# Optimization experiments

Measured on AMD Instinct MI355X. Metric: run time of the kernel, lower is better.

## Reference

```python
import jax, jax.numpy as jnp
import numpy as np

N_HEAD = 32
N_KV_HEAD = 8
HEAD_DIM = 64
N_EMBD = 2048
B, T = 2, 2048
ROPE_BASE = 10000.0


def _rope_cos_sin(T, head_dim, dtype):
    pos = jnp.arange(T, dtype=jnp.float32)
    dim_arr = jnp.arange(0, head_dim, 2, dtype=jnp.float32)
    freqs = ROPE_BASE ** (-dim_arr / head_dim)
    theta = jnp.outer(pos, freqs)                      # [T, hd/2]
    cos = jnp.concatenate([jnp.cos(theta), jnp.cos(theta)], axis=-1)  # [T, hd]
    sin = jnp.concatenate([jnp.sin(theta), jnp.sin(theta)], axis=-1)
    # broadcast to [1, T, 1, hd]
    return cos[None, :, None, :].astype(dtype), sin[None, :, None, :].astype(dtype)


def _rotate_half(v):
    h = v.shape[-1] // 2
    return jnp.concatenate([-v[..., h:], v[..., :h]], axis=-1)


def setup_inputs() -> dict:
    key = jax.random.key(0)
    kx, kq, kk, kv, ko = jax.random.split(key, 5)
    s = 1.0 / np.sqrt(N_EMBD)
    return {
        "x": jax.random.normal(kx, (B, T, N_EMBD), dtype=jnp.float32),
        "wq": jax.random.normal(kq, (N_EMBD, N_HEAD * HEAD_DIM), dtype=jnp.float32) * s,
        "wk": jax.random.normal(kk, (N_EMBD, N_KV_HEAD * HEAD_DIM), dtype=jnp.float32) * s,
        "wv": jax.random.normal(kv, (N_EMBD, N_KV_HEAD * HEAD_DIM), dtype=jnp.float32) * s,
        "wo": jax.random.normal(ko, (N_HEAD * HEAD_DIM, N_EMBD), dtype=jnp.float32) * s,
    }


def reference(x, wq, wk, wv, wo):
    Bx, Tx, C = x.shape
    n_rep = N_HEAD // N_KV_HEAD

    xq = (x @ wq).reshape(Bx, Tx, N_HEAD, HEAD_DIM)
    xk = (x @ wk).reshape(Bx, Tx, N_KV_HEAD, HEAD_DIM)
    xv = (x @ wv).reshape(Bx, Tx, N_KV_HEAD, HEAD_DIM)

    cos, sin = _rope_cos_sin(Tx, HEAD_DIM, x.dtype)
    xq = xq * cos + _rotate_half(xq) * sin
    xk = xk * cos + _rotate_half(xk) * sin

    # GQA: repeat_interleave KV heads to match query heads
    xk = jnp.repeat(xk, n_rep, axis=2)  # [B, T, H, hd]
    xv = jnp.repeat(xv, n_rep, axis=2)

    scale = 1.0 / np.sqrt(HEAD_DIM)
    # scores: [B, H, T, T]
    scores = jnp.einsum("bqhd,bkhd->bhqk", xq, xk) * scale
    causal = jnp.tril(jnp.ones((Tx, Tx), dtype=bool))
    scores = jnp.where(causal[None, None], scores, -jnp.inf)
    probs = jax.nn.softmax(scores, axis=-1)

    out = jnp.einsum("bhqk,bkhd->bqhd", probs, xv).reshape(Bx, Tx, N_HEAD * HEAD_DIM)
    return out @ wo
```

## Files before the change

kernel.cpp:

```cpp
#include <hip/hip_runtime.h>
#include <hip/hip_bf16.h>
#include <cstdint>
#include <cstddef>

#define B_ 2
#define T_ 2048
#define H_ 32
#define KVH_ 8
#define D_ 64
#define C_ 2048
#define NQKV 3072

typedef short short8 __attribute__((ext_vector_type(8)));
typedef float f32x4 __attribute__((ext_vector_type(4)));
typedef unsigned short u16;

__device__ __forceinline__ u16 f2b(float f) {
  union { float f; unsigned u; } x; x.f = f;
  unsigned r = x.u + 0x7fffu + ((x.u >> 16) & 1u);
  return (u16)(r >> 16);
}

__device__ __forceinline__ void gload16(const void* g, void* l) {
  __builtin_amdgcn_global_load_lds(
      (const __attribute__((address_space(1))) unsigned int*)g,
      (__attribute__((address_space(3))) unsigned int*)l,
      16, 0, 0);
}

__device__ __forceinline__ f32x4 mfma16(short8 a, short8 b, f32x4 c) {
  return __builtin_amdgcn_mfma_f32_16x16x32_bf16(a, b, c, 0, 0, 0);
}

__device__ __forceinline__ unsigned cvtpk(float lo_, float hi_) {
  unsigned r;
  asm("v_cvt_pk_bf16_f32 %0, %1, %2" : "=v"(r) : "v"(lo_), "v"(hi_));
  return r;
}

__global__ void k_tbl(float* __restrict__ tbl) {
  int i = blockIdx.x * 256 + threadIdx.x;
  int t = i >> 5, f = i & 31;
  double freq = pow(10000.0, -(double)f / 32.0);
  double th = (double)t * freq;
  tbl[i * 2 + 0] = (float)cos(th);
  tbl[i * 2 + 1] = (float)sin(th);
}

__global__ void k_cvtx(const float* __restrict__ x, u16* __restrict__ xb) {
  int i = blockIdx.x * 256 + threadIdx.x;
  float4 v = ((const float4*)x)[i];
  ushort4 o;
  o.x = f2b(v.x); o.y = f2b(v.y); o.z = f2b(v.z); o.w = f2b(v.w);
  ((ushort4*)xb)[i] = o;
}

__global__ void k_transw_qkv(const float* __restrict__ wq, const float* __restrict__ wk,
                             const float* __restrict__ wv, u16* __restrict__ dst) {
  __shared__ float t[32][33];
  int tx = threadIdx.x, ty = threadIdx.y;
  int k0 = blockIdx.y * 32, n0g = blockIdx.x * 32;
  const float* src;
  int N, col0;
  if (n0g < 2048)      { src = wq; N = 2048; col0 = n0g; }
  else if (n0g < 2560) { src = wk; N = 512;  col0 = n0g - 2048; }
  else                 { src = wv; N = 512;  col0 = n0g - 2560; }
#pragma unroll
  for (int i = 0; i < 4; i++)
    t[ty + i * 8][tx] = src[(size_t)(k0 + ty + i * 8) * N + col0 + tx];
  __syncthreads();
#pragma unroll
  for (int i = 0; i < 4; i++) {
    int nl = ty + i * 8;
    dst[(size_t)(n0g + nl) * 2048 + k0 + tx] = f2b(t[tx][nl]);
  }
}

__global__ void k_transw(const float* __restrict__ src, u16* __restrict__ dst, int N) {
  __shared__ float t[32][33];
  int tx = threadIdx.x, ty = threadIdx.y;
  int k0 = blockIdx.y * 32, n0 = blockIdx.x * 32;
#pragma unroll
  for (int i = 0; i < 4; i++)
    t[ty + i * 8][tx] = src[(size_t)(k0 + ty + i * 8) * N + n0 + tx];
  __syncthreads();
#pragma unroll
  for (int i = 0; i < 4; i++) {
    int nl = ty + i * 8;
    dst[(size_t)(n0 + nl) * 2048 + k0 + tx] = f2b(t[tx][nl]);
  }
}

template <int MODE>
__global__ __launch_bounds__(256, 2) void k_gemm(const u16* __restrict__ A,
                                                 const u16* __restrict__ Bt,
                                                 void* __restrict__ Cc,
                                                 int M, int N, int K,
                                                 const float* __restrict__ tbl,
                                                 u16* __restrict__ Qb,
                                                 u16* __restrict__ Kb,
                                                 u16* __restrict__ Vt) {
  __shared__ __align__(16) u16 As[128 * 64];
  __shared__ __align__(16) u16 Bs[128 * 64];
  const int tid = threadIdx.x;
  const int w = tid >> 6, l = tid & 63;
  const int lo = l & 15, hi = l >> 4;
  const int m0 = blockIdx.y * 128, n0 = blockIdx.x * 128;
  const int wr = w >> 1, wc = w & 1;
  f32x4 acc[4][4];
#pragma unroll
  for (int i = 0; i < 4; i++)
#pragma unroll
    for (int j = 0; j < 4; j++) acc[i][j] = (f32x4){0.f, 0.f, 0.f, 0.f};

  for (int k0 = 0; k0 < K; k0 += 64) {
#pragma unroll
    for (int i = 0; i < 4; i++) {
      int cid = i * 256 + tid;
      int row = cid >> 3, kc = cid & 7;
      gload16(A + (size_t)(m0 + row) * K + k0 + kc * 8, &As[(i * 256 + w * 64) * 8]);
      gload16(Bt + (size_t)(n0 + row) * K + k0 + kc * 8, &Bs[(i * 256 + w * 64) * 8]);
    }
    __syncthreads();
#pragma unroll
    for (int kk = 0; kk < 2; kk++) {
      short8 a[4], b[4];
#pragma unroll
      for (int i = 0; i < 4; i++)
        a[i] = *(const short8*)&As[(wr * 64 + i * 16 + lo) * 64 + kk * 32 + hi * 8];
#pragma unroll
      for (int j = 0; j < 4; j++)
        b[j] = *(const short8*)&Bs[(wc * 64 + j * 16 + lo) * 64 + kk * 32 + hi * 8];
#pragma unroll
      for (int i = 0; i < 4; i++)
#pragma unroll
        for (int j = 0; j < 4; j++) acc[i][j] = mfma16(a[i], b[j], acc[i][j]);
    }
    __syncthreads();
  }
  const int r0 = m0 + wr * 64, c0 = n0 + wc * 64;

  if (MODE == 0) {
#pragma unroll
    for (int i = 0; i < 4; i++)
#pragma unroll
      for (int j = 0; j < 4; j++) {
        f32x4 v = acc[i][j];
        int col = c0 + j * 16 + lo;
        int rw = r0 + i * 16 + hi * 4;
#pragma unroll
        for (int r = 0; r < 4; r++)
          ((float*)Cc)[(size_t)(rw + r) * N + col] = v[r];
      }
  } else {
    const int hd = c0 >> 6;
    const int b = m0 >> 11;
    if (hd < 40) {
      const bool isQ = (hd < 32);
      const float sc = isQ ? 0.125f * 1.44269504089f : 1.0f;
      u16* dst = isQ ? (Qb + (size_t)(b * H_ + hd) * T_ * 64)
                     : (Kb + (size_t)(b * KVH_ + (hd - 32)) * T_ * 64);
#pragma unroll
      for (int i = 0; i < 4; i++)
#pragma unroll
        for (int r = 0; r < 4; r++) {
          int t = (r0 + i * 16 + hi * 4 + r) & (T_ - 1);
          float2 cA = *(const float2*)&tbl[((size_t)t * 32 + lo) * 2];
          float2 cB = *(const float2*)&tbl[((size_t)t * 32 + 16 + lo) * 2];
          float a0 = acc[i][0][r], a1 = acc[i][1][r];
          float a2 = acc[i][2][r], a3 = acc[i][3][r];
          size_t rb = (size_t)t * 64;
          dst[rb + lo]      = f2b((a0 * cA.x - a2 * cA.y) * sc);
          dst[rb + 32 + lo] = f2b((a2 * cA.x + a0 * cA.y) * sc);
          dst[rb + 16 + lo] = f2b((a1 * cB.x - a3 * cB.y) * sc);
          dst[rb + 48 + lo] = f2b((a3 * cB.x + a1 * cB.y) * sc);
        }
    } else {
      const int kvh = hd - 40;
      u16* dst = Vt + (size_t)(b * KVH_ + kvh) * 64 * T_;
#pragma unroll
      for (int i = 0; i < 4; i++)
#pragma unroll
        for (int j = 0; j < 4; j++) {
          int t = (r0 + i * 16 + hi * 4) & (T_ - 1);
          int dd = j * 16 + lo;
          f32x4 v = acc[i][j];
          ushort4 ov;
          ov.x = f2b(v[0]); ov.y = f2b(v[1]); ov.z = f2b(v[2]); ov.w = f2b(v[3]);
          *(ushort4*)&dst[(size_t)dd * T_ + t] = ov;
        }
    }
  }
}

#define PSTR 40
__global__ __launch_bounds__(256)
__attribute__((amdgpu_waves_per_eu(3, 3)))
void k_attn(const u16* __restrict__ Qb,
            const u16* __restrict__ Kb,
            const u16* __restrict__ Vt,
            u16* __restrict__ Ob) {
  __shared__ __align__(16) u16 Pl[4][2][16 * PSTR];
  const int tid = threadIdx.x, w = tid >> 6, l = tid & 63;
  const int lo = l & 15, hi = l >> 4;
  const int b = blockIdx.z, h = blockIdx.y, kvh = h >> 2;
  const int p = (int)blockIdx.x * 4 + w;

  const size_t qbase = (size_t)(b * H_ + h) * T_ * 64;
  const size_t kbase = (size_t)(b * KVH_ + kvh) * T_ * 64;
  const size_t vbase = (size_t)(b * KVH_ + kvh) * 64 * T_;

  auto LOADK = [&](short8 (&ak)[2][2], int kv0) {
#pragma unroll
    for (int f = 0; f < 2; f++)
#pragma unroll
      for (int hf = 0; hf < 2; hf++)
        ak[f][hf] = *(const short8*)&Kb[kbase + (size_t)(kv0 + f * 16 + lo) * 64 + hf * 32 + hi * 8];
  };

  for (int pass = 0; pass < 2; pass++) {
    const int tile = pass ? (63 - p) : p;
    const int q0 = tile * 32;

    short8 aq[2][2];
#pragma unroll
    for (int qt = 0; qt < 2; qt++)
#pragma unroll
      for (int hf = 0; hf < 2; hf++)
        aq[qt][hf] = *(const short8*)&Qb[qbase + (size_t)(q0 + qt * 16 + lo) * 64 + hf * 32 + hi * 8];

    f32x4 o[2][4];
    float m[2], lsum[2];
#pragma unroll
    for (int qt = 0; qt < 2; qt++) {
      m[qt] = -1e30f; lsum[qt] = 0.f;
#pragma unroll
      for (int jd = 0; jd < 4; jd++) o[qt][jd] = (f32x4){0.f, 0.f, 0.f, 0.f};
    }

    auto STEP = [&](const short8 (&ak)[2][2], int kv0, bool masked) {
      short8 av[4];
#pragma unroll
      for (int jd = 0; jd < 4; jd++)
        av[jd] = *(const short8*)&Vt[vbase + (size_t)(jd * 16 + lo) * T_ + kv0 + hi * 8];

      f32x4 s[2][2];
      __builtin_amdgcn_s_setprio(1);
#pragma unroll
      for (int qt = 0; qt < 2; qt++)
#pragma unroll
        for (int f = 0; f < 2; f++) {
          f32x4 acc = (f32x4){0.f, 0.f, 0.f, 0.f};
          acc = mfma16(ak[f][0], aq[qt][0], acc);
          acc = mfma16(ak[f][1], aq[qt][1], acc);
          s[qt][f] = acc;
        }
      __builtin_amdgcn_s_setprio(0);

#pragma unroll
      for (int qt = 0; qt < 2; qt++) {
        const int myq = q0 + qt * 16 + lo;
        float p_[8];
#pragma unroll
        for (int f = 0; f < 2; f++)
#pragma unroll
          for (int r = 0; r < 4; r++) {
            float v = s[qt][f][r];
            if (masked) {
              int kv = kv0 + f * 16 + hi * 4 + r;
              v = (kv <= myq) ? v : -1e30f;
            }
            p_[f * 4 + r] = v;
          }
        float mx = fmaxf(fmaxf(fmaxf(p_[0], p_[1]), fmaxf(p_[2], p_[3])),
                         fmaxf(fmaxf(p_[4], p_[5]), fmaxf(p_[6], p_[7])));
        mx = fmaxf(mx, __shfl_xor(mx, 16));
        mx = fmaxf(mx, __shfl_xor(mx, 32));
        if (!__all(mx <= m[qt] + 11.5f)) {
          float mn = fmaxf(m[qt], mx);
          float a_ = exp2f(m[qt] - mn);
          m[qt] = mn;
          lsum[qt] *= a_;
#pragma unroll
          for (int jd = 0; jd < 4; jd++) {
            f32x4 t = o[qt][jd];
#pragma unroll
            for (int r = 0; r < 4; r++) t[r] *= a_;
            o[qt][jd] = t;
          }
        }
        float sm = 0.f;
#pragma unroll
        for (int i = 0; i < 8; i++) { p_[i] = exp2f(p_[i] - m[qt]); sm += p_[i]; }
        sm += __shfl_xor(sm, 16);
        sm += __shfl_xor(sm, 32);
        lsum[qt] += sm;
        uint2 w0, w1;
        w0.x = cvtpk(p_[0], p_[1]); w0.y = cvtpk(p_[2], p_[3]);
        w1.x = cvtpk(p_[4], p_[5]); w1.y = cvtpk(p_[6], p_[7]);
        *(uint2*)&Pl[w][qt][lo * PSTR + hi * 4] = w0;
        *(uint2*)&Pl[w][qt][lo * PSTR + 16 + hi * 4] = w1;
      }

#pragma unroll
      for (int qt = 0; qt < 2; qt++) {
        short8 pb = *(const short8*)&Pl[w][qt][lo * PSTR + hi * 8];
        __builtin_amdgcn_s_setprio(1);
#pragma unroll
        for (int jd = 0; jd < 4; jd++) o[qt][jd] = mfma16(av[jd], pb, o[qt][jd]);
        __builtin_amdgcn_s_setprio(0);
      }
    };

    short8 akA[2][2], akB[2][2];
    LOADK(akA, 0);
    int kv0 = 0;
    while (kv0 + 64 <= q0) {
      LOADK(akB, kv0 + 32);
      STEP(akA, kv0, false);
      LOADK(akA, kv0 + 64);
      STEP(akB, kv0 + 32, false);
      kv0 += 64;
    }
    if (kv0 < q0) {
      LOADK(akB, q0);
      STEP(akA, kv0, false);
      STEP(akB, q0, true);
    } else {
      STEP(akA, q0, true);
    }

#pragma unroll
    for (int qt = 0; qt < 2; qt++) {
      const int myq = q0 + qt * 16 + lo;
      float inv = 1.0f / lsum[qt];
      size_t obase = ((size_t)(b * T_ + myq) * H_ + h) * 64;
#pragma unroll
      for (int jd = 0; jd < 4; jd++) {
        ushort4 ov;
        ov.x = f2b(o[qt][jd][0] * inv);
        ov.y = f2b(o[qt][jd][1] * inv);
        ov.z = f2b(o[qt][jd][2] * inv);
        ov.w = f2b(o[qt][jd][3] * inv);
        *(ushort4*)&Ob[obase + jd * 16 + hi * 4] = ov;
      }
    }
  }
}

constexpr size_t OFF_TBL = 0;
constexpr size_t SZ_TBL = (size_t)T_ * 32 * 2 * 4;
constexpr size_t OFF_XB = OFF_TBL + SZ_TBL;
constexpr size_t SZ_XB = (size_t)B_ * T_ * C_ * 2;
constexpr size_t OFF_WQKVT = OFF_XB + SZ_XB;
constexpr size_t SZ_WQKVT = (size_t)NQKV * C_ * 2;
constexpr size_t OFF_WOT = OFF_WQKVT + SZ_WQKVT;
constexpr size_t SZ_WOT = (size_t)C_ * C_ * 2;
constexpr size_t OFF_QB = OFF_WOT + SZ_WOT;
constexpr size_t SZ_QB = (size_t)B_ * H_ * T_ * D_ * 2;
constexpr size_t OFF_KB = OFF_QB + SZ_QB;
constexpr size_t SZ_KVB = (size_t)B_ * KVH_ * T_ * D_ * 2;
constexpr size_t OFF_VT = OFF_KB + SZ_KVB;
constexpr size_t OFF_OB = OFF_VT + SZ_KVB;
constexpr size_t SZ_OB = (size_t)B_ * T_ * H_ * D_ * 2;

extern "C" void kernel_launch(void* const* d_in, const int* in_sizes, int n_in,
                              void* d_out, int out_size, void* d_ws, size_t ws_size,
                              hipStream_t stream) {
  const float* x = (const float*)d_in[0];
  const float* wq = (const float*)d_in[1];
  const float* wk = (const float*)d_in[2];
  const float* wv = (const float*)d_in[3];
  const float* wo = (const float*)d_in[4];

  char* ws = (char*)d_ws;
  float* tbl = (float*)(ws + OFF_TBL);
  u16* xb = (u16*)(ws + OFF_XB);
  u16* wqkvT = (u16*)(ws + OFF_WQKVT);
  u16* woT = (u16*)(ws + OFF_WOT);
  u16* Qb = (u16*)(ws + OFF_QB);
  u16* Kb = (u16*)(ws + OFF_KB);
  u16* Vt = (u16*)(ws + OFF_VT);
  u16* Ob = (u16*)(ws + OFF_OB);

  k_tbl<<<256, 256, 0, stream>>>(tbl);
  k_cvtx<<<8192, 256, 0, stream>>>(x, xb);
  dim3 tb(32, 8);
  k_transw_qkv<<<dim3(96, 64), tb, 0, stream>>>(wq, wk, wv, wqkvT);
  k_transw<<<dim3(64, 64), tb, 0, stream>>>(wo, woT, 2048);

  k_gemm<1><<<dim3(NQKV / 128, (B_ * T_) / 128), 256, 0, stream>>>(
      xb, wqkvT, nullptr, B_ * T_, NQKV, C_, tbl, Qb, Kb, Vt);
  k_attn<<<dim3(8, H_, B_), 256, 0, stream>>>(Qb, Kb, Vt, Ob);
  k_gemm<0><<<dim3(C_ / 128, (B_ * T_) / 128), 256, 0, stream>>>(
      Ob, woT, d_out, B_ * T_, C_, C_, nullptr, nullptr, nullptr, nullptr);
}
```

Baseline: 260.3 us.

## Split attention KV range across waves with LDS combine of partial softmax

```diff
diff --git a/kernel.cpp b/kernel.cpp
--- a/kernel.cpp
+++ b/kernel.cpp
@@ -200,16 +200,43 @@
             const u16* __restrict__ Kb,
             const u16* __restrict__ Vt,
             u16* __restrict__ Ob) {
-  __shared__ __align__(16) u16 Pl[4][2][16 * PSTR];
+  __shared__ __align__(16) char lds[17408];
+  u16* Pl = (u16*)lds;
+  f32x4* cbO0 = (f32x4*)lds;
+  f32x4* cbO1 = (f32x4*)(lds + 8192);
+  float* cbM = (float*)(lds + 16384);
+  float* cbL = cbM + 128;
+
   const int tid = threadIdx.x, w = tid >> 6, l = tid & 63;
   const int lo = l & 15, hi = l >> 4;
-  const int b = blockIdx.z, h = blockIdx.y, kvh = h >> 2;
-  const int p = (int)blockIdx.x * 4 + w;
+  const int bh = blockIdx.x;
+  const int b = bh >> 5, h = bh & 31, kvh = h >> 2;
+  const int tile = 63 - (int)blockIdx.y;
+  const int q0 = tile * 32;
+  const int nblk = tile + 1;
+  const int s0 = (nblk * w) >> 2;
+  const int s1 = (nblk * (w + 1)) >> 2;
 
   const size_t qbase = (size_t)(b * H_ + h) * T_ * 64;
   const size_t kbase = (size_t)(b * KVH_ + kvh) * T_ * 64;
   const size_t vbase = (size_t)(b * KVH_ + kvh) * 64 * T_;
 
+  short8 aq[2][2];
+#pragma unroll
+  for (int qt = 0; qt < 2; qt++)
+#pragma unroll
+    for (int hf = 0; hf < 2; hf++)
+      aq[qt][hf] = *(const short8*)&Qb[qbase + (size_t)(q0 + qt * 16 + lo) * 64 + hf * 32 + hi * 8];
+
+  f32x4 o[2][4];
+  float m[2], lsum[2];
+#pragma unroll
+  for (int qt = 0; qt < 2; qt++) {
+    m[qt] = -1e30f; lsum[qt] = 0.f;
+#pragma unroll
+    for (int jd = 0; jd < 4; jd++) o[qt][jd] = (f32x4){0.f, 0.f, 0.f, 0.f};
+  }
+
   auto LOADK = [&](short8 (&ak)[2][2], int kv0) {
 #pragma unroll
     for (int f = 0; f < 2; f++)
@@ -218,130 +245,169 @@
         ak[f][hf] = *(const short8*)&Kb[kbase + (size_t)(kv0 + f * 16 + lo) * 64 + hf * 32 + hi * 8];
   };
 
-  for (int pass = 0; pass < 2; pass++) {
-    const int tile = pass ? (63 - p) : p;
-    const int q0 = tile * 32;
-
-    short8 aq[2][2];
-#pragma unroll
-    for (int qt = 0; qt < 2; qt++)
-#pragma unroll
-      for (int hf = 0; hf < 2; hf++)
-        aq[qt][hf] = *(const short8*)&Qb[qbase + (size_t)(q0 + qt * 16 + lo) * 64 + hf * 32 + hi * 8];
-
-    f32x4 o[2][4];
-    float m[2], lsum[2];
-#pragma unroll
-    for (int qt = 0; qt < 2; qt++) {
-      m[qt] = -1e30f; lsum[qt] = 0.f;
-#pragma unroll
-      for (int jd = 0; jd < 4; jd++) o[qt][jd] = (f32x4){0.f, 0.f, 0.f, 0.f};
-    }
-
-    auto STEP = [&](const short8 (&ak)[2][2], int kv0, bool masked) {
-      short8 av[4];
-#pragma unroll
-      for (int jd = 0; jd < 4; jd++)
-        av[jd] = *(const short8*)&Vt[vbase + (size_t)(jd * 16 + lo) * T_ + kv0 + hi * 8];
-
-      f32x4 s[2][2];
-      __builtin_amdgcn_s_setprio(1);
-#pragma unroll
-      for (int qt = 0; qt < 2; qt++)
-#pragma unroll
-        for (int f = 0; f < 2; f++) {
-          f32x4 acc = (f32x4){0.f, 0.f, 0.f, 0.f};
-          acc = mfma16(ak[f][0], aq[qt][0], acc);
-          acc = mfma16(ak[f][1], aq[qt][1], acc);
-          s[qt][f] = acc;
-        }
-      __builtin_amdgcn_s_setprio(0);
-
-#pragma unroll
-      for (int qt = 0; qt < 2; qt++) {
-        const int myq = q0 + qt * 16 + lo;
-        float p_[8];
-#pragma unroll
-        for (int f = 0; f < 2; f++)
-#pragma unroll
-          for (int r = 0; r < 4; r++) {
-            float v = s[qt][f][r];
-            if (masked) {
-              int kv = kv0 + f * 16 + hi * 4 + r;
-              v = (kv <= myq) ? v : -1e30f;
-            }
-            p_[f * 4 + r] = v;
-          }
-        float mx = fmaxf(fmaxf(fmaxf(p_[0], p_[1]), fmaxf(p_[2], p_[3])),
-                         fmaxf(fmaxf(p_[4], p_[5]), fmaxf(p_[6], p_[7])));
-        mx = fmaxf(mx, __shfl_xor(mx, 16));
-        mx = fmaxf(mx, __shfl_xor(mx, 32));
-        if (!__all(mx <= m[qt] + 11.5f)) {
-          float mn = fmaxf(m[qt], mx);
-          float a_ = exp2f(m[qt] - mn);
-          m[qt] = mn;
-          lsum[qt] *= a_;
-#pragma unroll
-          for (int jd = 0; jd < 4; jd++) {
-            f32x4 t = o[qt][jd];
-#pragma unroll
-            for (int r = 0; r < 4; r++) t[r] *= a_;
-            o[qt][jd] = t;
-          }
-        }
-        float sm = 0.f;
-#pragma unroll
-        for (int i = 0; i < 8; i++) { p_[i] = exp2f(p_[i] - m[qt]); sm += p_[i]; }
-        sm += __shfl_xor(sm, 16);
-        sm += __shfl_xor(sm, 32);
-        lsum[qt] += sm;
-        uint2 w0, w1;
-        w0.x = cvtpk(p_[0], p_[1]); w0.y = cvtpk(p_[2], p_[3]);
-        w1.x = cvtpk(p_[4], p_[5]); w1.y = cvtpk(p_[6], p_[7]);
-        *(uint2*)&Pl[w][qt][lo * PSTR + hi * 4] = w0;
-        *(uint2*)&Pl[w][qt][lo * PSTR + 16 + hi * 4] = w1;
+  auto STEP = [&](const short8 (&ak)[2][2], int kv0, bool masked) {
+    short8 av[4];
+#pragma unroll
+    for (int jd = 0; jd < 4; jd++)
+      av[jd] = *(const short8*)&Vt[vbase + (size_t)(jd * 16 + lo) * T_ + kv0 + hi * 8];
+
+    f32x4 s[2][2];
+    __builtin_amdgcn_s_setprio(1);
+#pragma unroll
+    for (int qt = 0; qt < 2; qt++)
+#pragma unroll
+      for (int f = 0; f < 2; f++) {
+        f32x4 acc = (f32x4){0.f, 0.f, 0.f, 0.f};
+        acc = mfma16(ak[f][0], aq[qt][0], acc);
+        acc = mfma16(ak[f][1], aq[qt][1], acc);
+        s[qt][f] = acc;
       }
-
-#pragma unroll
-      for (int qt = 0; qt < 2; qt++) {
-        short8 pb = *(const short8*)&Pl[w][qt][lo * PSTR + hi * 8];
-        __builtin_amdgcn_s_setprio(1);
-#pragma unroll
-        for (int jd = 0; jd < 4; jd++) o[qt][jd] = mfma16(av[jd], pb, o[qt][jd]);
-        __builtin_amdgcn_s_setprio(0);
-      }
-    };
-
-    short8 akA[2][2], akB[2][2];
-    LOADK(akA, 0);
-    int kv0 = 0;
-    while (kv0 + 64 <= q0) {
-      LOADK(akB, kv0 + 32);
-      STEP(akA, kv0, false);
-      LOADK(akA, kv0 + 64);
-      STEP(akB, kv0 + 32, false);
-      kv0 += 64;
-    }
-    if (kv0 < q0) {
-      LOADK(akB, q0);
-      STEP(akA, kv0, false);
-      STEP(akB, q0, true);
-    } else {
-      STEP(akA, q0, true);
-    }
+    __builtin_amdgcn_s_setprio(0);
 
 #pragma unroll
     for (int qt = 0; qt < 2; qt++) {
       const int myq = q0 + qt * 16 + lo;
-      float inv = 1.0f / lsum[qt];
+      float p_[8];
+#pragma unroll
+      for (int f = 0; f < 2; f++)
+#pragma unroll
+        for (int r = 0; r < 4; r++) {
+          float v = s[qt][f][r];
+          if (masked) {
+            int kv = kv0 + f * 16 + hi * 4 + r;
+            v = (kv <= myq) ? v : -1e30f;
+          }
+          p_[f * 4 + r] = v;
+        }
+      float mx = fmaxf(fmaxf(fmaxf(p_[0], p_[1]), fmaxf(p_[2], p_[3])),
+                       fmaxf(fmaxf(p_[4], p_[5]), fmaxf(p_[6], p_[7])));
+      mx = fmaxf(mx, __shfl_xor(mx, 16));
+      mx = fmaxf(mx, __shfl_xor(mx, 32));
+      if (!__all(mx <= m[qt] + 11.5f)) {
+        float mn = fmaxf(m[qt], mx);
+        float a_ = exp2f(m[qt] - mn);
+        m[qt] = mn;
+        lsum[qt] *= a_;
+#pragma unroll
+        for (int jd = 0; jd < 4; jd++) {
+          f32x4 t = o[qt][jd];
+#pragma unroll
+          for (int r = 0; r < 4; r++) t[r] *= a_;
+          o[qt][jd] = t;
+        }
+      }
+      float sm = 0.f;
+#pragma unroll
+      for (int i = 0; i < 8; i++) { p_[i] = exp2f(p_[i] - m[qt]); sm += p_[i]; }
+      sm += __shfl_xor(sm, 16);
+      sm += __shfl_xor(sm, 32);
+      lsum[qt] += sm;
+      uint2 w0, w1;
+      w0.x = cvtpk(p_[0], p_[1]); w0.y = cvtpk(p_[2], p_[3]);
+      w1.x = cvtpk(p_[4], p_[5]); w1.y = cvtpk(p_[6], p_[7]);
+      *(uint2*)&Pl[((w * 2 + qt) * 16 + lo) * PSTR + hi * 4] = w0;
+      *(uint2*)&Pl[((w * 2 + qt) * 16 + lo) * PSTR + 16 + hi * 4] = w1;
+    }
+
+#pragma unroll
+    for (int qt = 0; qt < 2; qt++) {
+      short8 pb = *(const short8*)&Pl[((w * 2 + qt) * 16 + lo) * PSTR + hi * 8];
+      __builtin_amdgcn_s_setprio(1);
+#pragma unroll
+      for (int jd = 0; jd < 4; jd++) o[qt][jd] = mfma16(av[jd], pb, o[qt][jd]);
+      __builtin_amdgcn_s_setprio(0);
+    }
+  };
+
+  if (s0 < s1) {
+    short8 akA[2][2], akB[2][2];
+    int kb = s0;
+    LOADK(akA, kb * 32);
+    while (kb + 2 <= s1) {
+      LOADK(akB, (kb + 1) * 32);
+      STEP(akA, kb * 32, false);
+      if (kb + 2 < s1) LOADK(akA, (kb + 2) * 32);
+      STEP(akB, (kb + 1) * 32, (kb + 1) == nblk - 1);
+      kb += 2;
+    }
+    if (kb < s1) STEP(akA, kb * 32, kb == nblk - 1);
+  }
+
+  if (hi == 0) {
+#pragma unroll
+    for (int qt = 0; qt < 2; qt++) {
+      cbM[(w * 2 + qt) * 16 + lo] = m[qt];
+      cbL[(w * 2 + qt) * 16 + lo] = lsum[qt];
+    }
+  }
+  __syncthreads();
+  float linv[2];
+#pragma unroll
+  for (int qt = 0; qt < 2; qt++) {
+    float m0 = cbM[(0 + qt) * 16 + lo], m1 = cbM[(2 + qt) * 16 + lo],
+          m2 = cbM[(4 + qt) * 16 + lo], m3 = cbM[(6 + qt) * 16 + lo];
+    float ms = fmaxf(fmaxf(m0, m1), fmaxf(m2, m3));
+    float lt = cbL[(0 + qt) * 16 + lo] * exp2f(m0 - ms) +
+               cbL[(2 + qt) * 16 + lo] * exp2f(m1 - ms) +
+               cbL[(4 + qt) * 16 + lo] * exp2f(m2 - ms) +
+               cbL[(6 + qt) * 16 + lo] * exp2f(m3 - ms);
+    float sw = exp2f(m[qt] - ms);
+    linv[qt] = 1.0f / lt;
+#pragma unroll
+    for (int jd = 0; jd < 4; jd++) {
+      f32x4 t = o[qt][jd];
+#pragma unroll
+      for (int r = 0; r < 4; r++) t[r] *= sw;
+      o[qt][jd] = t;
+    }
+  }
+  if (w == 1) {
+#pragma unroll
+    for (int qt = 0; qt < 2; qt++)
+#pragma unroll
+      for (int jd = 0; jd < 4; jd++) cbO0[(qt * 4 + jd) * 64 + l] = o[qt][jd];
+  }
+  if (w == 3) {
+#pragma unroll
+    for (int qt = 0; qt < 2; qt++)
+#pragma unroll
+      for (int jd = 0; jd < 4; jd++) cbO1[(qt * 4 + jd) * 64 + l] = o[qt][jd];
+  }
+  __syncthreads();
+  if (w == 0) {
+#pragma unroll
+    for (int qt = 0; qt < 2; qt++)
+#pragma unroll
+      for (int jd = 0; jd < 4; jd++) o[qt][jd] += cbO0[(qt * 4 + jd) * 64 + l];
+  }
+  if (w == 2) {
+#pragma unroll
+    for (int qt = 0; qt < 2; qt++)
+#pragma unroll
+      for (int jd = 0; jd < 4; jd++) o[qt][jd] += cbO1[(qt * 4 + jd) * 64 + l];
+  }
+  __syncthreads();
+  if (w == 2) {
+#pragma unroll
+    for (int qt = 0; qt < 2; qt++)
+#pragma unroll
+      for (int jd = 0; jd < 4; jd++) cbO0[(qt * 4 + jd) * 64 + l] = o[qt][jd];
+  }
+  __syncthreads();
+  if (w == 0) {
+#pragma unroll
+    for (int qt = 0; qt < 2; qt++) {
+      const int myq = q0 + qt * 16 + lo;
       size_t obase = ((size_t)(b * T_ + myq) * H_ + h) * 64;
 #pragma unroll
       for (int jd = 0; jd < 4; jd++) {
+        f32x4 t = o[qt][jd];
+        t += cbO0[(qt * 4 + jd) * 64 + l];
         ushort4 ov;
-        ov.x = f2b(o[qt][jd][0] * inv);
-        ov.y = f2b(o[qt][jd][1] * inv);
-        ov.z = f2b(o[qt][jd][2] * inv);
-        ov.w = f2b(o[qt][jd][3] * inv);
+        ov.x = f2b(t[0] * linv[qt]);
+        ov.y = f2b(t[1] * linv[qt]);
+        ov.z = f2b(t[2] * linv[qt]);
+        ov.w = f2b(t[3] * linv[qt]);
         *(ushort4*)&Ob[obase + jd * 16 + hi * 4] = ov;
       }
     }
@@ -391,7 +457,7 @@
 
   k_gemm<1><<<dim3(NQKV / 128, (B_ * T_) / 128), 256, 0, stream>>>(
       xb, wqkvT, nullptr, B_ * T_, NQKV, C_, tbl, Qb, Kb, Vt);
-  k_attn<<<dim3(8, H_, B_), 256, 0, stream>>>(Qb, Kb, Vt, Ob);
+  k_attn<<<dim3(64, 64), 256, 0, stream>>>(Qb, Kb, Vt, Ob);
   k_gemm<0><<<dim3(C_ / 128, (B_ * T_) / 128), 256, 0, stream>>>(
       Ob, woT, d_out, B_ * T_, C_, C_, nullptr, nullptr, nullptr, nullptr);
 }
```

New measurement: 265.1 us. About the same (+1.8%).
